# Performance work log

Measured on AMD Instinct MI355X. Metric: run time of the kernel, lower is better.

## Reference

```python
import jax, jax.numpy as jnp
import numpy as np

B, S, D, H, DM = 2, 2048, 1024, 16, 4
HD = D // H  # head_dim = 64
EPS = 1e-5


def setup_inputs() -> dict:
    key = jax.random.key(0)
    ks = jax.random.split(key, 8)
    s = 0.02
    return {
        "x": jax.random.normal(ks[0], (B, S, D), jnp.float32),
        "wq": jax.random.normal(ks[1], (D, D), jnp.float32) * s,
        "wk": jax.random.normal(ks[2], (D, D), jnp.float32) * s,
        "wv": jax.random.normal(ks[3], (D, D), jnp.float32) * s,
        "wo": jax.random.normal(ks[4], (D, D), jnp.float32) * s,
        "bo": jnp.zeros((D,), jnp.float32),
        "ln1_scale": jnp.ones((D,), jnp.float32),
        "ln1_shift": jnp.zeros((D,), jnp.float32),
        "ln2_scale": jnp.ones((D,), jnp.float32),
        "ln2_shift": jnp.zeros((D,), jnp.float32),
        "w1": jax.random.normal(ks[5], (DM * D, D), jnp.float32) * s,
        "b1": jnp.zeros((DM * D,), jnp.float32),
        "w2": jax.random.normal(ks[6], (D, DM * D), jnp.float32) * s,
        "b2": jnp.zeros((D,), jnp.float32),
    }


def _layernorm(x, scale, shift):
    mean = jnp.mean(x, axis=-1, keepdims=True)
    var = jnp.var(x, axis=-1, keepdims=True)  # unbiased=False
    return scale * (x - mean) * jax.lax.rsqrt(var + EPS) + shift


def _attn(x, wq, wk, wv, wo, bo):
    b, n, d = x.shape
    # torch Linear: y = x @ W.T
    q = (x @ wq.T).reshape(b, n, H, HD).transpose(0, 2, 1, 3)  # [b,h,n,hd]
    k = (x @ wk.T).reshape(b, n, H, HD).transpose(0, 2, 1, 3)
    v = (x @ wv.T).reshape(b, n, H, HD).transpose(0, 2, 1, 3)
    scores = jnp.einsum("bhqd,bhkd->bhqk", q, k)
    causal = jnp.tril(jnp.ones((n, n), bool))
    scores = jnp.where(causal, scores, -jnp.inf)
    w = jax.nn.softmax(scores / np.sqrt(HD).astype(np.float32), axis=-1)
    ctx = jnp.einsum("bhqk,bhkd->bhqd", w, v)
    ctx = ctx.transpose(0, 2, 1, 3).reshape(b, n, d)
    return ctx @ wo.T + bo


def reference(x, wq, wk, wv, wo, bo, ln1_scale, ln1_shift, ln2_scale, ln2_shift, w1, b1, w2, b2):
    h = x + _attn(_layernorm(x, ln1_scale, ln1_shift), wq, wk, wv, wo, bo)
    y = _layernorm(h, ln2_scale, ln2_shift)
    y = jax.nn.relu(y @ w1.T + b1) @ w2.T + b2
    return h + y
```

## Files before the change

kernel.cpp:

```cpp
#include <hip/hip_runtime.h>

#define DEV __device__ __forceinline__

typedef __attribute__((ext_vector_type(8))) short bf8;
typedef __attribute__((ext_vector_type(4))) float f4;
typedef __attribute__((ext_vector_type(16))) float f16x;

DEV unsigned short f2bf(float f) {
  unsigned int u = __float_as_uint(f);
  u += 0x7FFFu + ((u >> 16) & 1u);
  return (unsigned short)(u >> 16);
}
DEV unsigned int pk2(float a, float b) {
  return (unsigned int)f2bf(a) | ((unsigned int)f2bf(b) << 16);
}

DEV int2 swz_tile(int ob, int nxt, int nyt) {
  const int nb = nxt * nyt;
  const int cpx = nb >> 3;
  const int W = (ob & 7) * cpx + (ob >> 3);
  const int scw = 4 * nyt;
  const int sc = W / scw, rem = W - sc * scw;
  return make_int2(rem >> 2, sc * 4 + (rem & 3));
}

template<bool BIAS, bool RELU, bool OUTBF, bool WRVT>
__global__ __launch_bounds__(512, 2) void gemm_bt256(
    const unsigned short* __restrict__ A, const unsigned short* __restrict__ B,
    const float* __restrict__ bias, void* __restrict__ Cout,
    int M, int N, int K, int ldc, unsigned short* __restrict__ vtout, int nyt)
{
  __shared__ unsigned short Sl[2][2][256 * 64];
  const int t = threadIdx.x;
  const int w = t >> 6, l = t & 63;
  const int wr = w >> 2, wc = w & 3;
  int2 tt = swz_tile((int)blockIdx.x, N >> 8, nyt);
  const int m0 = tt.x * 256, n0 = tt.y * 256;

  const int srow = w * 32 + (l >> 3);
  const int scol = 8 * ((l & 7) ^ (l >> 3));
  const unsigned short* Ab = A + (size_t)(m0 + srow) * K + scol;
  const unsigned short* Bb = B + (size_t)(n0 + srow) * K + scol;
  const int sdst = w * 2048 + l * 8;

  auto STAGE = [&](int slot, int kt) {
#pragma unroll
    for (int i = 0; i < 4; ++i) {
      __builtin_amdgcn_global_load_lds(
          (const __attribute__((address_space(1))) void*)(Ab + (size_t)i * 8 * K + kt * 64),
          (__attribute__((address_space(3))) void*)(&Sl[slot][0][sdst + i * 512]), 16, 0, 0);
      __builtin_amdgcn_global_load_lds(
          (const __attribute__((address_space(1))) void*)(Bb + (size_t)i * 8 * K + kt * 64),
          (__attribute__((address_space(3))) void*)(&Sl[slot][1][sdst + i * 512]), 16, 0, 0);
    }
  };

  const f4 fz = {0.f, 0.f, 0.f, 0.f};
  f4 acc[8][4];
#pragma unroll
  for (int i = 0; i < 8; ++i)
#pragma unroll
    for (int j = 0; j < 4; ++j) acc[i][j] = fz;

  const int NT = K >> 6;
  STAGE(0, 0);
  __syncthreads();

  for (int T = 0; T < NT; ++T) {
    if (T + 1 < NT) STAGE((T + 1) & 1, T + 1);
    const int sl = T & 1;
#pragma unroll
    for (int ks = 0; ks < 2; ++ks) {
      const int cb = (ks * 64 + ((l >> 4) * 16)) ^ ((l & 7) << 4);
      bf8 af[8], bg[4];
#pragma unroll
      for (int m = 0; m < 8; ++m)
        af[m] = *(const bf8*)((const char*)&Sl[sl][0][(wr * 128 + m * 16 + (l & 15)) * 64] + cb);
#pragma unroll
      for (int n = 0; n < 4; ++n)
        bg[n] = *(const bf8*)((const char*)&Sl[sl][1][(wc * 64 + n * 16 + (l & 15)) * 64] + cb);
      __builtin_amdgcn_s_setprio(1);
#pragma unroll
      for (int m = 0; m < 8; ++m)
#pragma unroll
        for (int n = 0; n < 4; ++n)
          acc[m][n] = __builtin_amdgcn_mfma_f32_16x16x32_bf16(af[m], bg[n], acc[m][n], 0, 0, 0);
      __builtin_amdgcn_s_setprio(0);
    }
    __syncthreads();
  }

#pragma unroll
  for (int n = 0; n < 4; ++n) {
    const int col = n0 + wc * 64 + n * 16 + (l & 15);
    float bv = 0.f;
    if (BIAS) bv = bias[col];
    const bool isv = WRVT && (col >= 2048);
    const int hh = (col - 2048) >> 6, dd = (col - 2048) & 63;
#pragma unroll
    for (int m = 0; m < 8; ++m) {
#pragma unroll
      for (int r = 0; r < 4; ++r) {
        const int row = m0 + wr * 128 + m * 16 + ((l >> 4) * 4) + r;
        float v = acc[m][n][r] + bv;
        if (RELU) v = fmaxf(v, 0.f);
        if (WRVT && isv) {
          const int bb = row >> 11, ss = row & 2047;
          vtout[((size_t)(bb * 16 + hh) * 64 + dd) * 2048 + ss] = f2bf(v);
        } else if (OUTBF) {
          ((unsigned short*)Cout)[(size_t)row * ldc + col] = f2bf(v);
        } else {
          ((float*)Cout)[(size_t)row * ldc + col] = v;
        }
      }
    }
  }
}

template<bool BIAS, bool RELU, bool RESID, bool OUTBF>
__global__ __launch_bounds__(256) void gemm_bt(
    const unsigned short* __restrict__ A, const unsigned short* __restrict__ B,
    const float* __restrict__ bias, const float* __restrict__ resid,
    void* __restrict__ Cout, int M, int N, int K, int ldc, int nyt)
{
  __shared__ unsigned short Al[2][128 * 32];
  __shared__ unsigned short Bl[2][128 * 32];
  const int t = threadIdx.x;
  const int w = t >> 6, l = t & 63;
  const int wr = w >> 1, wc = w & 1;
  int2 tt = swz_tile((int)blockIdx.x, N >> 7, nyt);
  const int m0 = tt.x * 128, n0 = tt.y * 128;

  const int srow = w * 16 + (l >> 2);
  const int scsw = ((l & 3) * 8) ^ (((srow >> 1) & 3) << 3);
  const unsigned short* Ab = A + (size_t)(m0 + srow) * K + scsw;
  const unsigned short* Bb = B + (size_t)(n0 + srow) * K + scsw;
  const int sdst = w * 512 + l * 8;

  auto STAGE = [&](int slot, int k0) {
#pragma unroll
    for (int i = 0; i < 2; ++i) {
      __builtin_amdgcn_global_load_lds(
          (const __attribute__((address_space(1))) void*)(Ab + (size_t)i * 64 * K + k0),
          (__attribute__((address_space(3))) void*)(&Al[slot][sdst + i * 2048]), 16, 0, 0);
      __builtin_amdgcn_global_load_lds(
          (const __attribute__((address_space(1))) void*)(Bb + (size_t)i * 64 * K + k0),
          (__attribute__((address_space(3))) void*)(&Bl[slot][sdst + i * 2048]), 16, 0, 0);
    }
  };

  const f4 fz = {0.f, 0.f, 0.f, 0.f};
  f4 acc[4][4];
#pragma unroll
  for (int i = 0; i < 4; ++i)
#pragma unroll
    for (int j = 0; j < 4; ++j) acc[i][j] = fz;

  const int NT = K >> 5;
  STAGE(0, 0);
  __syncthreads();

  for (int T = 0; T < NT; ++T) {
    if (T + 1 < NT) STAGE((T + 1) & 1, (T + 1) * 32);
    const int sl = T & 1;
    const int rdcol = ((l >> 4) * 8) ^ ((((l & 15) >> 1) & 3) << 3);
    bf8 af[4], bg[4];
#pragma unroll
    for (int am = 0; am < 4; ++am)
      af[am] = *(const bf8*)&Al[sl][(wr * 64 + am * 16 + (l & 15)) * 32 + rdcol];
#pragma unroll
    for (int bn = 0; bn < 4; ++bn)
      bg[bn] = *(const bf8*)&Bl[sl][(wc * 64 + bn * 16 + (l & 15)) * 32 + rdcol];
    __builtin_amdgcn_s_setprio(1);
#pragma unroll
    for (int am = 0; am < 4; ++am)
#pragma unroll
      for (int bn = 0; bn < 4; ++bn)
        acc[am][bn] = __builtin_amdgcn_mfma_f32_16x16x32_bf16(af[am], bg[bn], acc[am][bn], 0, 0, 0);
    __builtin_amdgcn_s_setprio(0);
    __syncthreads();
  }

#pragma unroll
  for (int bn = 0; bn < 4; ++bn) {
    const int col = n0 + wc * 64 + bn * 16 + (l & 15);
    float bv = 0.f;
    if (BIAS) bv = bias[col];
#pragma unroll
    for (int am = 0; am < 4; ++am) {
#pragma unroll
      for (int r = 0; r < 4; ++r) {
        const int row = m0 + wr * 64 + am * 16 + ((l >> 4) * 4) + r;
        float v = acc[am][bn][r] + bv;
        if (RELU) v = fmaxf(v, 0.f);
        if (RESID) v += resid[(size_t)row * ldc + col];
        if (OUTBF) ((unsigned short*)Cout)[(size_t)row * ldc + col] = f2bf(v);
        else       ((float*)Cout)[(size_t)row * ldc + col] = v;
      }
    }
  }
}

__global__ __launch_bounds__(256, 2) void attn_kernel(
    const unsigned short* __restrict__ qk, const unsigned short* __restrict__ vt,
    unsigned short* __restrict__ ctx)
{
  __shared__ unsigned short Ks[2][64 * 64];
  __shared__ unsigned short Vs[2][64 * 64];

  const int t = threadIdx.x;
  const int w = t >> 6, l = t & 63;
  const int hi = l >> 5, q = l & 31;
  const int qt = 15 - (int)blockIdx.x;
  const int h = blockIdx.y, b = blockIdx.z;
  const int q0w = qt * 128 + w * 32;
  const unsigned short* qbase = qk + ((size_t)b * 2048) * 2048 + h * 64;
  const unsigned short* kbase = qbase + 1024;
  const unsigned short* vbase = vt + ((size_t)(b * 16 + h)) * 64 * 2048;

  bf8 qf[4];
#pragma unroll
  for (int ksl = 0; ksl < 4; ++ksl)
    qf[ksl] = *(const bf8*)(qbase + (size_t)(q0w + q) * 2048 + ksl * 16 + hi * 8);

  f16x oacc[2];
#pragma unroll
  for (int dn = 0; dn < 2; ++dn)
#pragma unroll
    for (int i = 0; i < 16; ++i) oacc[dn][i] = 0.f;
  float m_ = -1e30f, l_ = 0.f;

  const int nit = 2 * qt + 2;

  auto STAGE = [&](int buf, int it) {
#pragma unroll
    for (int s = 0; s < 2; ++s) {
      const int row = s * 32 + (t >> 3);
      const int cb = (t & 7) * 16;
      const int sb = cb ^ ((row & 7) << 4);
      __builtin_amdgcn_global_load_lds(
          (const __attribute__((address_space(1))) void*)
              (kbase + (size_t)(it * 64 + row) * 2048 + (sb >> 1)),
          (__attribute__((address_space(3))) void*)(&Ks[buf][row * 64 + (cb >> 1)]),
          16, 0, 0);
      __builtin_amdgcn_global_load_lds(
          (const __attribute__((address_space(1))) void*)
              (vbase + (size_t)row * 2048 + it * 64 + (sb >> 1)),
          (__attribute__((address_space(3))) void*)(&Vs[buf][row * 64 + (cb >> 1)]),
          16, 0, 0);
    }
  };

  STAGE(0, 0);
  __syncthreads();

  for (int it = 0; it < nit; ++it) {
    const int buf = it & 1;
    if (it + 1 < nit) STAGE(buf ^ 1, it + 1);
    const int kb0 = it * 64;

    if (kb0 <= q0w + 31) {
      const bool bdry = (kb0 + 63) > q0w;
#pragma unroll
      for (int sg = 0; sg < 2; ++sg) {
        f16x sacc;
#pragma unroll
        for (int i = 0; i < 16; ++i) sacc[i] = 0.f;
#pragma unroll
        for (int ksl = 0; ksl < 4; ++ksl) {
          const int row = sg * 32 + q;
          const int cb = ((ksl * 16 + hi * 8) * 2) ^ ((row & 7) << 4);
          bf8 kf = *(const bf8*)((const char*)&Ks[buf][row * 64] + cb);
          sacc = __builtin_amdgcn_mfma_f32_32x32x16_bf16(kf, qf[ksl], sacc, 0, 0, 0);
        }
        float p[16];
        if (bdry) {
#pragma unroll
          for (int i = 0; i < 16; ++i) {
            const int key = kb0 + sg * 32 + (i & 3) + 8 * (i >> 2) + 4 * hi;
            p[i] = (key <= q0w + q) ? sacc[i] : -1e30f;
          }
        } else {
#pragma unroll
          for (int i = 0; i < 16; ++i) p[i] = sacc[i];
        }
        float mx = p[0];
#pragma unroll
        for (int i = 1; i < 16; ++i) mx = fmaxf(mx, p[i]);
        mx = fmaxf(mx, __shfl_xor(mx, 32));
        const float mn = fmaxf(m_, mx);
        const float alpha = __expf(m_ - mn);
        m_ = mn;
        float rs = 0.f;
#pragma unroll
        for (int i = 0; i < 16; ++i) { p[i] = __expf(p[i] - mn); rs += p[i]; }
        rs += __shfl_xor(rs, 32);
        l_ = alpha * l_ + rs;
#pragma unroll
        for (int dn = 0; dn < 2; ++dn)
#pragma unroll
          for (int i = 0; i < 16; ++i) oacc[dn][i] *= alpha;

        unsigned int wds[8];
#pragma unroll
        for (int m = 0; m < 4; ++m) {
          wds[m * 2]     = pk2(p[4 * m], p[4 * m + 1]);
          wds[m * 2 + 1] = pk2(p[4 * m + 2], p[4 * m + 3]);
        }
#pragma unroll
        for (int kq = 0; kq < 2; ++kq) {
          unsigned int x0 = __shfl_xor((int)(hi ? wds[4 * kq]     : wds[4 * kq + 2]), 32);
          unsigned int x1 = __shfl_xor((int)(hi ? wds[4 * kq + 1] : wds[4 * kq + 3]), 32);
          unsigned int pw0 = hi ? x0 : wds[4 * kq];
          unsigned int pw1 = hi ? x1 : wds[4 * kq + 1];
          unsigned int pw2 = hi ? wds[4 * kq + 2] : x0;
          unsigned int pw3 = hi ? wds[4 * kq + 3] : x1;
          union { unsigned int u[4]; bf8 v; } pu;
          pu.u[0] = pw0; pu.u[1] = pw1; pu.u[2] = pw2; pu.u[3] = pw3;
          const bf8 pf = pu.v;
#pragma unroll
          for (int dn = 0; dn < 2; ++dn) {
            const int row = dn * 32 + q;
            const int cb = ((sg * 32 + kq * 16 + hi * 8) * 2) ^ ((row & 7) << 4);
            bf8 vf = *(const bf8*)((const char*)&Vs[buf][row * 64] + cb);
            oacc[dn] = __builtin_amdgcn_mfma_f32_32x32x16_bf16(vf, pf, oacc[dn], 0, 0, 0);
          }
        }
      }
    }
    __syncthreads();
  }

  const float inv = 1.0f / l_;
  unsigned short* crow = ctx + ((size_t)(b * 2048 + q0w + q)) * 1024 + h * 64;
#pragma unroll
  for (int dn = 0; dn < 2; ++dn)
#pragma unroll
    for (int m = 0; m < 4; ++m) {
      const int d0 = dn * 32 + 8 * m + 4 * hi;
      *(unsigned int*)(crow + d0)     = pk2(oacc[dn][4 * m] * inv, oacc[dn][4 * m + 1] * inv);
      *(unsigned int*)(crow + d0 + 2) = pk2(oacc[dn][4 * m + 2] * inv, oacc[dn][4 * m + 3] * inv);
    }
}

__global__ __launch_bounds__(256) void ln_kernel(
    const float* __restrict__ x, const float* __restrict__ sc,
    const float* __restrict__ sh, unsigned short* __restrict__ out)
{
  const int row = blockIdx.x, t = threadIdx.x;
  float4 v = ((const float4*)x)[(size_t)row * 256 + t];
  float s = v.x + v.y + v.z + v.w;
  float q = v.x * v.x + v.y * v.y + v.z * v.z + v.w * v.w;
#pragma unroll
  for (int off = 1; off < 64; off <<= 1) {
    s += __shfl_xor(s, off);
    q += __shfl_xor(q, off);
  }
  __shared__ float red[8];
  const int w = t >> 6, l = t & 63;
  if (l == 0) { red[w] = s; red[4 + w] = q; }
  __syncthreads();
  s = red[0] + red[1] + red[2] + red[3];
  q = red[4] + red[5] + red[6] + red[7];
  const float mean = s * (1.0f / 1024.0f);
  const float var = q * (1.0f / 1024.0f) - mean * mean;
  const float rstd = rsqrtf(var + 1e-5f);
  float4 scv = ((const float4*)sc)[t];
  float4 shv = ((const float4*)sh)[t];
  uint2 p;
  p.x = pk2(scv.x * (v.x - mean) * rstd + shv.x, scv.y * (v.y - mean) * rstd + shv.y);
  p.y = pk2(scv.z * (v.z - mean) * rstd + shv.z, scv.w * (v.w - mean) * rstd + shv.w);
  ((uint2*)out)[(size_t)row * 256 + t] = p;
}

__global__ __launch_bounds__(256) void cvt_kernel(
    const float* __restrict__ src, unsigned short* __restrict__ dst,
    int n4, float scale)
{
  int i = blockIdx.x * 256 + threadIdx.x;
  const int stride = gridDim.x * 256;
  for (; i < n4; i += stride) {
    float4 v = ((const float4*)src)[i];
    uint2 p;
    p.x = pk2(v.x * scale, v.y * scale);
    p.y = pk2(v.z * scale, v.w * scale);
    ((uint2*)dst)[i] = p;
  }
}

extern "C" void kernel_launch(void* const* d_in, const int* in_sizes, int n_in,
                              void* d_out, int out_size, void* d_ws, size_t ws_size,
                              hipStream_t stream)
{
  const float* x    = (const float*)d_in[0];
  const float* wq   = (const float*)d_in[1];
  const float* wk   = (const float*)d_in[2];
  const float* wv   = (const float*)d_in[3];
  const float* wo   = (const float*)d_in[4];
  const float* bo   = (const float*)d_in[5];
  const float* ln1s = (const float*)d_in[6];
  const float* ln1b = (const float*)d_in[7];
  const float* ln2s = (const float*)d_in[8];
  const float* ln2b = (const float*)d_in[9];
  const float* w1   = (const float*)d_in[10];
  const float* b1   = (const float*)d_in[11];
  const float* w2   = (const float*)d_in[12];
  const float* b2   = (const float*)d_in[13];
  float* out = (float*)d_out;

  const int M = 4096;

  unsigned short* ws   = (unsigned short*)d_ws;
  unsigned short* lnb  = ws;
  unsigned short* qkvw = lnb  + (size_t)4096 * 1024;
  unsigned short* wob  = qkvw + (size_t)3072 * 1024;
  unsigned short* w1b  = wob  + (size_t)1024 * 1024;
  unsigned short* w2b  = w1b  + (size_t)4096 * 1024;
  unsigned short* qkb  = w2b  + (size_t)4096 * 1024;
  unsigned short* vtb  = qkb  + (size_t)4096 * 2048;
  unsigned short* ctxb = vtb  + (size_t)32 * 64 * 2048;
  float* hf = (float*)(ctxb + (size_t)4096 * 1024);

  cvt_kernel<<<1024, 256, 0, stream>>>(wq, qkvw,                       (1024 * 1024) / 4, 0.125f);
  cvt_kernel<<<1024, 256, 0, stream>>>(wk, qkvw + (size_t)1024 * 1024, (1024 * 1024) / 4, 1.0f);
  cvt_kernel<<<1024, 256, 0, stream>>>(wv, qkvw + (size_t)2048 * 1024, (1024 * 1024) / 4, 1.0f);
  cvt_kernel<<<1024, 256, 0, stream>>>(wo, wob,                        (1024 * 1024) / 4, 1.0f);
  cvt_kernel<<<2048, 256, 0, stream>>>(w1, w1b, (4096 * 1024) / 4, 1.0f);
  cvt_kernel<<<2048, 256, 0, stream>>>(w2, w2b, (4096 * 1024) / 4, 1.0f);

  ln_kernel<<<M, 256, 0, stream>>>(x, ln1s, ln1b, lnb);
  gemm_bt256<false, false, true, true><<<192, 512, 0, stream>>>(
      lnb, qkvw, nullptr, qkb, M, 3072, 1024, 2048, vtb, 16);
  attn_kernel<<<dim3(16, 16, 2), 256, 0, stream>>>(qkb, vtb, ctxb);
  gemm_bt<true, false, true, false><<<256, 256, 0, stream>>>(
      ctxb, wob, bo, x, hf, M, 1024, 1024, 1024, 32);
  ln_kernel<<<M, 256, 0, stream>>>(hf, ln2s, ln2b, lnb);
  gemm_bt256<true, true, true, false><<<256, 512, 0, stream>>>(
      lnb, w1b, b1, qkb, M, 4096, 1024, 4096, nullptr, 16);
  gemm_bt<true, false, true, false><<<256, 256, 0, stream>>>(
      qkb, w2b, b2, hf, out, M, 1024, 4096, 1024, 32);
}
```

Measured before the change: 286.3 us.

## Rebalance causal attention with paired query tiles and lazy rescaling; merge weight conversions

Attention blocks now use 128 threads and each processes two 64-row query tiles (j and 31-j), so every block does the same amount of causal work. The inner loop handles a full 64-key block per iteration and uses tree reductions for max and sum. Rescaling of the running output is skipped unless the new max exceeds the old by more than 8. The six weight-conversion launches become one kernel, and bf16 packing now uses HIP intrinsics. Risks are fewer waves per block, which may reduce latency hiding, and the lazy rescale threshold, which could affect numerical range.

```diff
diff --git a/kernel.cpp b/kernel.cpp
--- a/kernel.cpp
+++ b/kernel.cpp
@@ -1,4 +1,5 @@
 #include <hip/hip_runtime.h>
+#include <hip/hip_bf16.h>
 
 #define DEV __device__ __forceinline__
 
@@ -7,12 +8,14 @@
 typedef __attribute__((ext_vector_type(16))) float f16x;
 
 DEV unsigned short f2bf(float f) {
-  unsigned int u = __float_as_uint(f);
-  u += 0x7FFFu + ((u >> 16) & 1u);
-  return (unsigned short)(u >> 16);
+  union { __hip_bfloat16 h; unsigned short u; } c;
+  c.h = __float2bfloat16(f);
+  return c.u;
 }
 DEV unsigned int pk2(float a, float b) {
-  return (unsigned int)f2bf(a) | ((unsigned int)f2bf(b) << 16);
+  union { __hip_bfloat162 h; unsigned int u; } c;
+  c.h = __hip_bfloat162(__float2bfloat16(a), __float2bfloat16(b));
+  return c.u;
 }
 
 DEV int2 swz_tile(int ob, int nxt, int nyt) {
@@ -201,7 +204,7 @@
   }
 }
 
-__global__ __launch_bounds__(256, 2) void attn_kernel(
+__global__ __launch_bounds__(128, 2) void attn_kernel(
     const unsigned short* __restrict__ qk, const unsigned short* __restrict__ vt,
     unsigned short* __restrict__ ctx)
 {
@@ -211,31 +214,16 @@
   const int t = threadIdx.x;
   const int w = t >> 6, l = t & 63;
   const int hi = l >> 5, q = l & 31;
-  const int qt = 15 - (int)blockIdx.x;
+  const int j = blockIdx.x;
   const int h = blockIdx.y, b = blockIdx.z;
-  const int q0w = qt * 128 + w * 32;
   const unsigned short* qbase = qk + ((size_t)b * 2048) * 2048 + h * 64;
   const unsigned short* kbase = qbase + 1024;
   const unsigned short* vbase = vt + ((size_t)(b * 16 + h)) * 64 * 2048;
 
-  bf8 qf[4];
-#pragma unroll
-  for (int ksl = 0; ksl < 4; ++ksl)
-    qf[ksl] = *(const bf8*)(qbase + (size_t)(q0w + q) * 2048 + ksl * 16 + hi * 8);
-
-  f16x oacc[2];
-#pragma unroll
-  for (int dn = 0; dn < 2; ++dn)
-#pragma unroll
-    for (int i = 0; i < 16; ++i) oacc[dn][i] = 0.f;
-  float m_ = -1e30f, l_ = 0.f;
-
-  const int nit = 2 * qt + 2;
-
   auto STAGE = [&](int buf, int it) {
 #pragma unroll
-    for (int s = 0; s < 2; ++s) {
-      const int row = s * 32 + (t >> 3);
+    for (int s = 0; s < 4; ++s) {
+      const int row = s * 16 + (t >> 3);
       const int cb = (t & 7) * 16;
       const int sb = cb ^ ((row & 7) << 4);
       __builtin_amdgcn_global_load_lds(
@@ -251,72 +239,105 @@
     }
   };
 
-  STAGE(0, 0);
-  __syncthreads();
-
-  for (int it = 0; it < nit; ++it) {
-    const int buf = it & 1;
-    if (it + 1 < nit) STAGE(buf ^ 1, it + 1);
-    const int kb0 = it * 64;
-
-    if (kb0 <= q0w + 31) {
-      const bool bdry = (kb0 + 63) > q0w;
-#pragma unroll
-      for (int sg = 0; sg < 2; ++sg) {
-        f16x sacc;
-#pragma unroll
-        for (int i = 0; i < 16; ++i) sacc[i] = 0.f;
-#pragma unroll
-        for (int ksl = 0; ksl < 4; ++ksl) {
-          const int row = sg * 32 + q;
-          const int cb = ((ksl * 16 + hi * 8) * 2) ^ ((row & 7) << 4);
-          bf8 kf = *(const bf8*)((const char*)&Ks[buf][row * 64] + cb);
-          sacc = __builtin_amdgcn_mfma_f32_32x32x16_bf16(kf, qf[ksl], sacc, 0, 0, 0);
+  for (int pass = 0; pass < 2; ++pass) {
+    const int qtile = pass ? j : 31 - j;
+    const int q0w = qtile * 64 + w * 32;
+    bf8 qf[4];
+#pragma unroll
+    for (int ksl = 0; ksl < 4; ++ksl)
+      qf[ksl] = *(const bf8*)(qbase + (size_t)(q0w + q) * 2048 + ksl * 16 + hi * 8);
+
+    f16x oacc[2];
+#pragma unroll
+    for (int dn = 0; dn < 2; ++dn)
+#pragma unroll
+      for (int i = 0; i < 16; ++i) oacc[dn][i] = 0.f;
+    float m_ = -1e30f, l_ = 0.f;
+
+    const int nit = qtile + 1;
+    STAGE(0, 0);
+    __syncthreads();
+
+    for (int it = 0; it < nit; ++it) {
+      const int buf = it & 1;
+      if (it + 1 < nit) STAGE(buf ^ 1, it + 1);
+      const int kb0 = it * 64;
+
+      f16x s0, s1;
+#pragma unroll
+      for (int i = 0; i < 16; ++i) { s0[i] = 0.f; s1[i] = 0.f; }
+#pragma unroll
+      for (int ksl = 0; ksl < 4; ++ksl) {
+        const int cbq = ((ksl * 16 + hi * 8) * 2);
+        const int r0 = q, r1 = 32 + q;
+        bf8 k0 = *(const bf8*)((const char*)&Ks[buf][r0 * 64] + (cbq ^ ((r0 & 7) << 4)));
+        bf8 k1 = *(const bf8*)((const char*)&Ks[buf][r1 * 64] + (cbq ^ ((r1 & 7) << 4)));
+        s0 = __builtin_amdgcn_mfma_f32_32x32x16_bf16(k0, qf[ksl], s0, 0, 0, 0);
+        s1 = __builtin_amdgcn_mfma_f32_32x32x16_bf16(k1, qf[ksl], s1, 0, 0, 0);
+      }
+
+      float p[32];
+      if (kb0 + 63 > q0w) {
+#pragma unroll
+        for (int i = 0; i < 16; ++i) {
+          const int key = kb0 + (i & 3) + 8 * (i >> 2) + 4 * hi;
+          p[i]      = (key <= q0w + q)      ? s0[i] : -1e30f;
+          p[16 + i] = (key + 32 <= q0w + q) ? s1[i] : -1e30f;
         }
-        float p[16];
-        if (bdry) {
-#pragma unroll
-          for (int i = 0; i < 16; ++i) {
-            const int key = kb0 + sg * 32 + (i & 3) + 8 * (i >> 2) + 4 * hi;
-            p[i] = (key <= q0w + q) ? sacc[i] : -1e30f;
-          }
-        } else {
-#pragma unroll
-          for (int i = 0; i < 16; ++i) p[i] = sacc[i];
-        }
-        float mx = p[0];
-#pragma unroll
-        for (int i = 1; i < 16; ++i) mx = fmaxf(mx, p[i]);
-        mx = fmaxf(mx, __shfl_xor(mx, 32));
-        const float mn = fmaxf(m_, mx);
+      } else {
+#pragma unroll
+        for (int i = 0; i < 16; ++i) { p[i] = s0[i]; p[16 + i] = s1[i]; }
+      }
+
+      float tm[16];
+#pragma unroll
+      for (int i = 0; i < 16; ++i) tm[i] = fmaxf(p[i], p[16 + i]);
+#pragma unroll
+      for (int st = 8; st >= 1; st >>= 1)
+#pragma unroll
+        for (int i = 0; i < 8; ++i)
+          if (i < st) tm[i] = fmaxf(tm[i], tm[i + st]);
+      const float pmax = fmaxf(tm[0], __shfl_xor(tm[0], 32));
+      if (__any(pmax > m_ + 8.0f)) {
+        const float mn = fmaxf(m_, pmax);
         const float alpha = __expf(m_ - mn);
         m_ = mn;
-        float rs = 0.f;
-#pragma unroll
-        for (int i = 0; i < 16; ++i) { p[i] = __expf(p[i] - mn); rs += p[i]; }
-        rs += __shfl_xor(rs, 32);
-        l_ = alpha * l_ + rs;
+        l_ *= alpha;
 #pragma unroll
         for (int dn = 0; dn < 2; ++dn)
 #pragma unroll
           for (int i = 0; i < 16; ++i) oacc[dn][i] *= alpha;
-
+      }
+#pragma unroll
+      for (int i = 0; i < 32; ++i) p[i] = __expf(p[i] - m_);
+      float ts[16];
+#pragma unroll
+      for (int i = 0; i < 16; ++i) ts[i] = p[i] + p[16 + i];
+#pragma unroll
+      for (int st = 8; st >= 1; st >>= 1)
+#pragma unroll
+        for (int i = 0; i < 8; ++i)
+          if (i < st) ts[i] += ts[i + st];
+      l_ += ts[0] + __shfl_xor(ts[0], 32);
+
+#pragma unroll
+      for (int sg = 0; sg < 2; ++sg) {
+        const float* pp = p + sg * 16;
         unsigned int wds[8];
 #pragma unroll
         for (int m = 0; m < 4; ++m) {
-          wds[m * 2]     = pk2(p[4 * m], p[4 * m + 1]);
-          wds[m * 2 + 1] = pk2(p[4 * m + 2], p[4 * m + 3]);
+          wds[m * 2]     = pk2(pp[4 * m], pp[4 * m + 1]);
+          wds[m * 2 + 1] = pk2(pp[4 * m + 2], pp[4 * m + 3]);
         }
 #pragma unroll
         for (int kq = 0; kq < 2; ++kq) {
           unsigned int x0 = __shfl_xor((int)(hi ? wds[4 * kq]     : wds[4 * kq + 2]), 32);
           unsigned int x1 = __shfl_xor((int)(hi ? wds[4 * kq + 1] : wds[4 * kq + 3]), 32);
-          unsigned int pw0 = hi ? x0 : wds[4 * kq];
-          unsigned int pw1 = hi ? x1 : wds[4 * kq + 1];
-          unsigned int pw2 = hi ? wds[4 * kq + 2] : x0;
-          unsigned int pw3 = hi ? wds[4 * kq + 3] : x1;
           union { unsigned int u[4]; bf8 v; } pu;
-          pu.u[0] = pw0; pu.u[1] = pw1; pu.u[2] = pw2; pu.u[3] = pw3;
+          pu.u[0] = hi ? x0 : wds[4 * kq];
+          pu.u[1] = hi ? x1 : wds[4 * kq + 1];
+          pu.u[2] = hi ? wds[4 * kq + 2] : x0;
+          pu.u[3] = hi ? wds[4 * kq + 3] : x1;
           const bf8 pf = pu.v;
 #pragma unroll
           for (int dn = 0; dn < 2; ++dn) {
@@ -327,20 +348,20 @@
           }
         }
       }
-    }
-    __syncthreads();
-  }
-
-  const float inv = 1.0f / l_;
-  unsigned short* crow = ctx + ((size_t)(b * 2048 + q0w + q)) * 1024 + h * 64;
-#pragma unroll
-  for (int dn = 0; dn < 2; ++dn)
-#pragma unroll
-    for (int m = 0; m < 4; ++m) {
-      const int d0 = dn * 32 + 8 * m + 4 * hi;
-      *(unsigned int*)(crow + d0)     = pk2(oacc[dn][4 * m] * inv, oacc[dn][4 * m + 1] * inv);
-      *(unsigned int*)(crow + d0 + 2) = pk2(oacc[dn][4 * m + 2] * inv, oacc[dn][4 * m + 3] * inv);
-    }
+      __syncthreads();
+    }
+
+    const float inv = 1.0f / l_;
+    unsigned short* crow = ctx + ((size_t)(b * 2048 + q0w + q)) * 1024 + h * 64;
+#pragma unroll
+    for (int dn = 0; dn < 2; ++dn)
+#pragma unroll
+      for (int m = 0; m < 4; ++m) {
+        const int d0 = dn * 32 + 8 * m + 4 * hi;
+        *(unsigned int*)(crow + d0)     = pk2(oacc[dn][4 * m] * inv, oacc[dn][4 * m + 1] * inv);
+        *(unsigned int*)(crow + d0 + 2) = pk2(oacc[dn][4 * m + 2] * inv, oacc[dn][4 * m + 3] * inv);
+      }
+  }
 }
 
 __global__ __launch_bounds__(256) void ln_kernel(
@@ -373,18 +394,35 @@
   ((uint2*)out)[(size_t)row * 256 + t] = p;
 }
 
-__global__ __launch_bounds__(256) void cvt_kernel(
-    const float* __restrict__ src, unsigned short* __restrict__ dst,
-    int n4, float scale)
-{
-  int i = blockIdx.x * 256 + threadIdx.x;
+__global__ __launch_bounds__(256) void cvt_weights(
+    const float* __restrict__ wq, const float* __restrict__ wk,
+    const float* __restrict__ wv, const float* __restrict__ wo,
+    const float* __restrict__ w1, const float* __restrict__ w2,
+    unsigned short* __restrict__ dst)
+{
+  const int M1 = 1 << 20;
+  const int n4 = (12 * M1) / 4;
   const int stride = gridDim.x * 256;
-  for (; i < n4; i += stride) {
-    float4 v = ((const float4*)src)[i];
-    uint2 p;
-    p.x = pk2(v.x * scale, v.y * scale);
-    p.y = pk2(v.z * scale, v.w * scale);
-    ((uint2*)dst)[i] = p;
+  for (int i4 = blockIdx.x * 256 + threadIdx.x; i4 < n4; i4 += stride) {
+    const size_t i = (size_t)i4 * 4;
+    const int mi = (int)(i >> 20);
+    const float* src;
+    size_t off;
+    float sc = 1.0f;
+    if (mi < 4) {
+      src = mi == 0 ? wq : mi == 1 ? wk : mi == 2 ? wv : wo;
+      off = i & (size_t)(M1 - 1);
+      if (mi == 0) sc = 0.125f;
+    } else if (mi < 8) {
+      src = w1; off = i - (size_t)4 * M1;
+    } else {
+      src = w2; off = i - (size_t)8 * M1;
+    }
+    float4 v = *(const float4*)(src + off);
+    uint2 pq;
+    pq.x = pk2(v.x * sc, v.y * sc);
+    pq.y = pk2(v.z * sc, v.w * sc);
+    ((uint2*)dst)[i4] = pq;
   }
 }
 
@@ -421,17 +459,12 @@
   unsigned short* ctxb = vtb  + (size_t)32 * 64 * 2048;
   float* hf = (float*)(ctxb + (size_t)4096 * 1024);
 
-  cvt_kernel<<<1024, 256, 0, stream>>>(wq, qkvw,                       (1024 * 1024) / 4, 0.125f);
-  cvt_kernel<<<1024, 256, 0, stream>>>(wk, qkvw + (size_t)1024 * 1024, (1024 * 1024) / 4, 1.0f);
-  cvt_kernel<<<1024, 256, 0, stream>>>(wv, qkvw + (size_t)2048 * 1024, (1024 * 1024) / 4, 1.0f);
-  cvt_kernel<<<1024, 256, 0, stream>>>(wo, wob,                        (1024 * 1024) / 4, 1.0f);
-  cvt_kernel<<<2048, 256, 0, stream>>>(w1, w1b, (4096 * 1024) / 4, 1.0f);
-  cvt_kernel<<<2048, 256, 0, stream>>>(w2, w2b, (4096 * 1024) / 4, 1.0f);
+  cvt_weights<<<2048, 256, 0, stream>>>(wq, wk, wv, wo, w1, w2, qkvw);
 
   ln_kernel<<<M, 256, 0, stream>>>(x, ln1s, ln1b, lnb);
   gemm_bt256<false, false, true, true><<<192, 512, 0, stream>>>(
       lnb, qkvw, nullptr, qkb, M, 3072, 1024, 2048, vtb, 16);
-  attn_kernel<<<dim3(16, 16, 2), 256, 0, stream>>>(qkb, vtb, ctxb);
+  attn_kernel<<<dim3(16, 16, 2), 128, 0, stream>>>(qkb, vtb, ctxb);
   gemm_bt<true, false, true, false><<<256, 256, 0, stream>>>(
       ctxb, wob, bo, x, hf, M, 1024, 1024, 1024, 32);
   ln_kernel<<<M, 256, 0, stream>>>(hf, ln2s, ln2b, lnb);
```

Result: faster. 272.6 us (-4.8%).
